# Performance work log

Measured on AMD Instinct MI355X. Metric: run time of the kernel, lower is better.

The kernel has to match this reference:

```python
import jax, jax.numpy as jnp
import numpy as np
import math

EMBED_DIM = 1024
NUM_HEADS = 16
HEAD_DIM = EMBED_DIM // NUM_HEADS          # 64
SUB_HEAD_DIM = HEAD_DIM // 2               # 32
SCALING = 1.0 / math.sqrt(SUB_HEAD_DIM)
LAMBDA_INIT = 0.8 - 0.6 * math.exp(-0.3 * 0)  # layer_idx = 0 -> 0.2


def setup_inputs() -> dict:
    key = jax.random.key(0)
    ks = jax.random.split(key, 10)
    B, T, D = 2, 2048, EMBED_DIM
    xav = math.sqrt(6.0 / (D + D))  # xavier_uniform bound for square-ish mats
    return {
        "query": jax.random.normal(ks[0], (B, T, D), jnp.float32),
        "key": jax.random.normal(ks[1], (B, T, D), jnp.float32),
        "value": jax.random.normal(ks[2], (B, T, D), jnp.float32),
        "in_proj_weight": jax.random.uniform(ks[3], (3 * D, D), jnp.float32, -xav, xav),
        "in_proj_bias": jnp.zeros((3 * D,), jnp.float32),
        "out_proj_weight": jax.random.uniform(ks[4], (D, D), jnp.float32, -xav, xav),
        "out_proj_bias": jnp.zeros((D,), jnp.float32),
        "lambda_q1": 0.1 * jax.random.normal(ks[5], (SUB_HEAD_DIM,), jnp.float32),
        "lambda_k1": 0.1 * jax.random.normal(ks[6], (SUB_HEAD_DIM,), jnp.float32),
        "lambda_q2": 0.1 * jax.random.normal(ks[7], (SUB_HEAD_DIM,), jnp.float32),
        "lambda_k2": 0.1 * jax.random.normal(ks[8], (SUB_HEAD_DIM,), jnp.float32),
    }


def reference(query, key, value, in_proj_weight, in_proj_bias,
              out_proj_weight, out_proj_bias,
              lambda_q1, lambda_k1, lambda_q2, lambda_k2):
    B, T, D = query.shape
    S = key.shape[1]
    H, hd, sd = NUM_HEADS, HEAD_DIM, SUB_HEAD_DIM

    qw, kw, vw = jnp.split(in_proj_weight, 3, axis=0)
    qb, kb, vb = jnp.split(in_proj_bias, 3, axis=0)
    q = query @ qw.T + qb
    k = key @ kw.T + kb
    v = value @ vw.T + vb

    # [B, H, T, head_dim]
    q = q.reshape(B, T, H, hd).transpose(0, 2, 1, 3)
    k = k.reshape(B, S, H, hd).transpose(0, 2, 1, 3)
    v = v.reshape(B, S, H, hd).transpose(0, 2, 1, 3)

    q1, q2 = q[..., :sd], q[..., sd:]
    k1, k2 = k[..., :sd], k[..., sd:]

    logits_1 = jnp.einsum('bhtd,bhsd->bhts', q1, k1) * SCALING
    logits_2 = jnp.einsum('bhtd,bhsd->bhts', q2, k2) * SCALING

    a1 = jax.nn.softmax(logits_1, axis=-1)
    a2 = jax.nn.softmax(logits_2, axis=-1)

    lam = (jnp.exp(jnp.dot(lambda_q1, lambda_k1))
           - jnp.exp(jnp.dot(lambda_q2, lambda_k2)) + LAMBDA_INIT)

    diff_weights = a1 - lam * a2
    attn_output = jnp.einsum('bhts,bhsd->bhtd', diff_weights, v)
    attn_output = attn_output * (1.0 - LAMBDA_INIT)

    attn_output = attn_output.transpose(0, 2, 1, 3).reshape(B, T, D)
    output = attn_output @ out_proj_weight.T + out_proj_bias
    return output
```

## Files before the change

### kernel.cpp

```cpp
#include <hip/hip_runtime.h>
#include <cstdint>
#include <cstddef>

typedef unsigned short u16;
typedef __attribute__((ext_vector_type(8))) short bf16x8;
typedef __attribute__((ext_vector_type(4))) short bf16x4;
typedef __attribute__((ext_vector_type(4))) float f32x4;

__device__ __forceinline__ u16 f2bf(float f) {
  uint32_t u = __float_as_uint(f);
  u += 0x7fffu + ((u >> 16) & 1u);
  return (u16)(u >> 16);
}

__device__ __forceinline__ short f2bfs(float f) {
  __bf16 h = (__bf16)f;
  return __builtin_bit_cast(short, h);
}

__device__ __forceinline__ float bf2f(u16 u) {
  return __uint_as_float(((uint32_t)u) << 16);
}

#define MFMA16(a, b, c) __builtin_amdgcn_mfma_f32_16x16x32_bf16((a), (b), (c), 0, 0, 0)

__device__ __forceinline__ float ex2(float x) {
#if __has_builtin(__builtin_amdgcn_exp2f)
  return __builtin_amdgcn_exp2f(x);
#else
  return exp2f(x);
#endif
}

__global__ __launch_bounds__(256) void cvt5_kernel(const float* __restrict__ q,
                                                   const float* __restrict__ k,
                                                   const float* __restrict__ v,
                                                   const float* __restrict__ w0,
                                                   const float* __restrict__ w1,
                                                   u16* __restrict__ X,
                                                   u16* __restrict__ Wqkv,
                                                   u16* __restrict__ Wout,
                                                   int n8i, int n8w, int n8o) {
  int i = blockIdx.x * blockDim.x + threadIdx.x;
  const int y = blockIdx.y;
  const float* src;
  u16* dst;
  if (y < 3) {
    if (i >= n8i) return;
    src = (y == 0) ? q : (y == 1 ? k : v);
    dst = X + (size_t)y * n8i * 8;
  } else if (y == 3) {
    if (i >= n8w) return;
    src = w0; dst = Wqkv;
  } else {
    if (i >= n8o) return;
    src = w1; dst = Wout;
  }
  const float4* p = (const float4*)src;
  float4 a = p[i * 2], b = p[i * 2 + 1];
  u16 o[8] = {f2bf(a.x), f2bf(a.y), f2bf(a.z), f2bf(a.w),
              f2bf(b.x), f2bf(b.y), f2bf(b.z), f2bf(b.w)};
  *(int4*)(dst + (size_t)i * 8) = *(const int4*)o;
}

__global__ __launch_bounds__(256) void gemm_qkv(const u16* __restrict__ Abase,
                                                const u16* __restrict__ B,
                                                const float* __restrict__ bias,
                                                u16* __restrict__ QH, u16* __restrict__ KH,
                                                u16* __restrict__ VT,
                                                int M, int N, int K) {
  __shared__ u16 As[128][68];
  __shared__ u16 Bs[128][68];
  const int nb = blockIdx.x, mb = blockIdx.y;
  const int t = threadIdx.x;
  const u16* A = Abase + (size_t)(nb >> 3) * (size_t)M * K;
  const int w = t >> 6, lane = t & 63;
  const int wr = w >> 1, wc = w & 1;
  const int lr = lane & 15, lk = lane >> 4;
  const f32x4 zero4 = {0.f, 0.f, 0.f, 0.f};
  f32x4 acc[4][4];
#pragma unroll
  for (int i = 0; i < 4; ++i)
#pragma unroll
    for (int j = 0; j < 4; ++j) acc[i][j] = zero4;

  const int srow = t >> 3;
  const int scol = (t & 7) << 3;
  const u16* Ap = A + (size_t)(mb * 128 + srow) * K + scol;
  const u16* Bp = B + (size_t)(nb * 128 + srow) * K + scol;

  for (int k0 = 0; k0 < K; k0 += 64) {
    __syncthreads();
#pragma unroll
    for (int j = 0; j < 4; ++j) {
      *(int4*)&As[srow + 32 * j][scol] = *(const int4*)(Ap + (size_t)(32 * j) * K + k0);
      *(int4*)&Bs[srow + 32 * j][scol] = *(const int4*)(Bp + (size_t)(32 * j) * K + k0);
    }
    __syncthreads();
#pragma unroll
    for (int kk = 0; kk < 2; ++kk) {
      bf16x8 af[4], bfr[4];
#pragma unroll
      for (int mf = 0; mf < 4; ++mf)
        af[mf] = *(const bf16x8*)&As[wr * 64 + mf * 16 + lr][kk * 32 + lk * 8];
#pragma unroll
      for (int nf = 0; nf < 4; ++nf)
        bfr[nf] = *(const bf16x8*)&Bs[wc * 64 + nf * 16 + lr][kk * 32 + lk * 8];
#pragma unroll
      for (int mf = 0; mf < 4; ++mf)
#pragma unroll
        for (int nf = 0; nf < 4; ++nf) acc[mf][nf] = MFMA16(af[mf], bfr[nf], acc[mf][nf]);
    }
  }

  const int third = nb >> 3;
  const int bb = mb >> 4;
#pragma unroll
  for (int nf = 0; nf < 4; ++nf) {
    const int col = nb * 128 + wc * 64 + nf * 16 + lr;
    const int c = col & 1023;
    const int h = c >> 6, d = c & 63;
    const float bv = bias[col];
    u16* qk = (third == 0 ? QH : KH) + (size_t)(bb * 16 + h) * 2048 * 64;
    u16* vt = VT + ((size_t)(bb * 16 + h) * 64 + d) * 2048;
#pragma unroll
    for (int mf = 0; mf < 4; ++mf) {
      const int row0 = mb * 128 + wr * 64 + mf * 16 + lk * 4;
      const int s0 = row0 & 2047;
      if (third < 2) {
#pragma unroll
        for (int r = 0; r < 4; ++r)
          qk[(size_t)(s0 + r) * 64 + d] = f2bf(acc[mf][nf][r] + bv);
      } else {
        u16 tmp[4];
#pragma unroll
        for (int r = 0; r < 4; ++r) tmp[r] = f2bf(acc[mf][nf][r] + bv);
        *(uint2*)&vt[s0] = *(const uint2*)tmp;
      }
    }
  }
}

__global__ __launch_bounds__(256) void gemm_out(const u16* __restrict__ A,
                                                const u16* __restrict__ B,
                                                const float* __restrict__ bias,
                                                float* __restrict__ C,
                                                int M, int N, int K) {
  __shared__ u16 As[128][68];
  __shared__ u16 Bs[64][68];
  const int nb = blockIdx.x, mb = blockIdx.y;
  const int t = threadIdx.x;
  const int w = t >> 6, lane = t & 63;
  const int lr = lane & 15, lk = lane >> 4;
  const f32x4 zero4 = {0.f, 0.f, 0.f, 0.f};
  f32x4 acc[2][4];
#pragma unroll
  for (int i = 0; i < 2; ++i)
#pragma unroll
    for (int j = 0; j < 4; ++j) acc[i][j] = zero4;

  const int srow = t >> 3;
  const int scol = (t & 7) << 3;
  const u16* Ap = A + (size_t)(mb * 128 + srow) * K + scol;
  const u16* Bp = B + (size_t)(nb * 64 + srow) * K + scol;

  for (int k0 = 0; k0 < K; k0 += 64) {
    __syncthreads();
#pragma unroll
    for (int j = 0; j < 4; ++j)
      *(int4*)&As[srow + 32 * j][scol] = *(const int4*)(Ap + (size_t)(32 * j) * K + k0);
#pragma unroll
    for (int j = 0; j < 2; ++j)
      *(int4*)&Bs[srow + 32 * j][scol] = *(const int4*)(Bp + (size_t)(32 * j) * K + k0);
    __syncthreads();
#pragma unroll
    for (int kk = 0; kk < 2; ++kk) {
      bf16x8 af[2], bfr[4];
#pragma unroll
      for (int mf = 0; mf < 2; ++mf)
        af[mf] = *(const bf16x8*)&As[w * 32 + mf * 16 + lr][kk * 32 + lk * 8];
#pragma unroll
      for (int nf = 0; nf < 4; ++nf)
        bfr[nf] = *(const bf16x8*)&Bs[nf * 16 + lr][kk * 32 + lk * 8];
#pragma unroll
      for (int mf = 0; mf < 2; ++mf)
#pragma unroll
        for (int nf = 0; nf < 4; ++nf) acc[mf][nf] = MFMA16(af[mf], bfr[nf], acc[mf][nf]);
    }
  }

#pragma unroll
  for (int nf = 0; nf < 4; ++nf) {
    const int col = nb * 64 + nf * 16 + lr;
    const float bv = bias[col];
#pragma unroll
    for (int mf = 0; mf < 2; ++mf) {
      const int row0 = mb * 128 + w * 32 + mf * 16 + lk * 4;
#pragma unroll
      for (int r = 0; r < 4; ++r)
        C[(size_t)(row0 + r) * N + col] = acc[mf][nf][r] + bv;
    }
  }
}

__global__ __launch_bounds__(512, 2) void diff_attn(const u16* __restrict__ QH,
                                                    const u16* __restrict__ KH,
                                                    const u16* __restrict__ VT,
                                                    const float* __restrict__ lq1,
                                                    const float* __restrict__ lk1,
                                                    const float* __restrict__ lq2,
                                                    const float* __restrict__ lk2,
                                                    u16* __restrict__ ATTN) {
  __shared__ u16 Ks[64][68];
  __shared__ u16 Vs[64][68];
  const int t = threadIdx.x;
  const int id = blockIdx.x;
  const int swz = (id & 7) * 64 + (id >> 3);
  const int qt = swz & 15, bh = swz >> 4;
  const int b = bh >> 4, h = bh & 15;
  const int w = t >> 6, lane = t & 63;
  const int lr = lane & 15, lk = lane >> 4;
  const float QSC = 0.17677669529663687f * 1.4426950408889634f;

  float dd1 = 0.f, dd2 = 0.f;
  for (int i = 0; i < 32; ++i) { dd1 += lq1[i] * lk1[i]; dd2 += lq2[i] * lk2[i]; }
  const float lam = __expf(dd1) - __expf(dd2) + 0.2f;

  const int srow = t >> 3;
  const int scol = (t & 7) << 3;
  const int krow = (srow & 32) | ((srow & 4) << 2) | ((srow & 24) >> 1) | (srow & 3);
  const u16* qh = QH + (size_t)(b * 16 + h) * 2048 * 64;
  const u16* kh = KH + (size_t)(b * 16 + h) * 2048 * 64;
  const u16* vt = VT + (size_t)(b * 16 + h) * 64 * 2048;

  bf16x8 qa[2];
#pragma unroll
  for (int hh = 0; hh < 2; ++hh) {
    bf16x8 q = *(const bf16x8*)(qh + (size_t)(qt * 128 + w * 16 + lr) * 64 + hh * 32 + lk * 8);
#pragma unroll
    for (int i = 0; i < 8; ++i) q[i] = f2bfs(bf2f((u16)q[i]) * QSC);
    qa[hh] = q;
  }

  const f32x4 zero4 = {0.f, 0.f, 0.f, 0.f};
  f32x4 O[2][4], Ol[2];
#pragma unroll
  for (int hh = 0; hh < 2; ++hh) {
    Ol[hh] = zero4;
#pragma unroll
    for (int df = 0; df < 4; ++df) O[hh][df] = zero4;
  }
  bf16x8 vone8;
#pragma unroll
  for (int i = 0; i < 8; ++i) vone8[i] = (short)0x3F80;

  const u16* kp = kh + (size_t)srow * 64 + scol;
  const u16* vp = vt + (size_t)srow * 2048 + scol;

  int4 kA = *(const int4*)kp;
  int4 vA = *(const int4*)vp;
  int4 kB, vB;

  for (int it = 0; it < 32; ++it) {
    __syncthreads();
    *(int4*)&Ks[krow][scol] = kA;
    *(int4*)&Vs[srow][scol] = vA;
    if (it < 31) {
      const int s1 = (it + 1) * 64;
      kB = *(const int4*)(kp + (size_t)s1 * 64);
      vB = *(const int4*)(vp + s1);
    }
    __syncthreads();

    bf16x8 pk8[2][2];
#pragma unroll
    for (int hh = 0; hh < 2; ++hh) {
      f32x4 St[4];
      __builtin_amdgcn_s_setprio(1);
#pragma unroll
      for (int nf = 0; nf < 4; ++nf) {
        bf16x8 kb = *(const bf16x8*)&Ks[nf * 16 + lr][hh * 32 + lk * 8];
        St[nf] = MFMA16(kb, qa[hh], zero4);
      }
      __builtin_amdgcn_s_setprio(0);
#pragma unroll
      for (int j = 0; j < 2; ++j) {
        bf16x8 p;
#pragma unroll
        for (int a = 0; a < 2; ++a)
#pragma unroll
          for (int r = 0; r < 4; ++r)
            p[a * 4 + r] = f2bfs(ex2(St[2 * j + a][r]));
        pk8[hh][j] = p;
      }
    }

    __builtin_amdgcn_s_setprio(1);
#pragma unroll
    for (int j = 0; j < 2; ++j) {
      const bf16x8 pa0 = pk8[0][j], pa1 = pk8[1][j];
#pragma unroll
      for (int df = 0; df < 4; ++df) {
        bf16x8 vb = *(const bf16x8*)&Vs[df * 16 + lr][j * 32 + lk * 8];
        O[0][df] = MFMA16(pa0, vb, O[0][df]);
        O[1][df] = MFMA16(pa1, vb, O[1][df]);
      }
      Ol[0] = MFMA16(pa0, vone8, Ol[0]);
      Ol[1] = MFMA16(pa1, vone8, Ol[1]);
    }
    __builtin_amdgcn_s_setprio(0);

    kA = kB; vA = vB;
  }

  float i1[4], i2[4];
#pragma unroll
  for (int r = 0; r < 4; ++r) {
    i1[r] = 1.f / Ol[0][r];
    i2[r] = 1.f / Ol[1][r];
  }
  const size_t qrow0 = (size_t)b * 2048 + (size_t)qt * 128;
#pragma unroll
  for (int df = 0; df < 4; ++df) {
    const int col = h * 64 + df * 16 + lr;
#pragma unroll
    for (int r = 0; r < 4; ++r) {
      const size_t row = qrow0 + w * 16 + lk * 4 + r;
      float v = 0.8f * (O[0][df][r] * i1[r] - lam * O[1][df][r] * i2[r]);
      ATTN[row * 1024 + col] = f2bf(v);
    }
  }
}

extern "C" void kernel_launch(void* const* d_in, const int* in_sizes, int n_in,
                              void* d_out, int out_size, void* d_ws, size_t ws_size,
                              hipStream_t stream) {
  (void)in_sizes; (void)n_in; (void)out_size; (void)ws_size;
  const float* query = (const float*)d_in[0];
  const float* key_  = (const float*)d_in[1];
  const float* value = (const float*)d_in[2];
  const float* ipw   = (const float*)d_in[3];
  const float* ipb   = (const float*)d_in[4];
  const float* opw   = (const float*)d_in[5];
  const float* opb   = (const float*)d_in[6];
  const float* lq1   = (const float*)d_in[7];
  const float* lk1   = (const float*)d_in[8];
  const float* lq2   = (const float*)d_in[9];
  const float* lk2   = (const float*)d_in[10];

  const int M = 4096, D = 1024;
  u16* X    = (u16*)d_ws;
  u16* Wqkv = X + (size_t)3 * M * D;
  u16* Wout = Wqkv + (size_t)3 * D * D;
  u16* QH   = Wout + (size_t)D * D;
  u16* KH   = QH + (size_t)M * D;
  u16* VT   = KH + (size_t)M * D;
  u16* ATTN = VT + (size_t)M * D;

  {
    int n8i = (int)((size_t)M * D / 8);
    int n8w = (int)((size_t)3 * D * D / 8);
    int n8o = (int)((size_t)D * D / 8);
    cvt5_kernel<<<dim3((n8i + 255) / 256, 5), dim3(256), 0, stream>>>(
        query, key_, value, ipw, opw, X, Wqkv, Wout, n8i, n8w, n8o);
  }

  gemm_qkv<<<dim3(24, 32), dim3(256), 0, stream>>>(
      X, Wqkv, ipb, QH, KH, VT, M, 3 * D, D);
  diff_attn<<<dim3(512), dim3(512), 0, stream>>>(QH, KH, VT, lq1, lk1, lq2, lk2, ATTN);
  gemm_out<<<dim3(16, 32), dim3(256), 0, stream>>>(
      ATTN, Wout, opb, (float*)d_out, M, D, D);
}
```

Baseline: 135.2 us.

## Use direct global-to-LDS loads in GEMMs and double attention KV tile

The QKV and output GEMMs now load tiles with global_load_lds, which writes straight into unpadded LDS instead of passing through registers, so the register round trip goes away. In exchange the LDS rows lose their padding and may suffer bank conflicts. The attention kernel now stages 128 keys per iteration instead of 64, which halves the number of barrier pairs and makes each prefetch larger, at the cost of more LDS and registers.

```diff
diff --git a/kernel.cpp b/kernel.cpp
--- a/kernel.cpp
+++ b/kernel.cpp
@@ -30,6 +30,12 @@
 #else
   return exp2f(x);
 #endif
+}
+
+__device__ __forceinline__ void gload_lds16(const u16* g, u16* l) {
+  __builtin_amdgcn_global_load_lds(
+      (const __attribute__((address_space(1))) unsigned int*)g,
+      (__attribute__((address_space(3))) unsigned int*)l, 16, 0, 0);
 }
 
 __global__ __launch_bounds__(256) void cvt5_kernel(const float* __restrict__ q,
@@ -69,8 +75,8 @@
                                                 u16* __restrict__ QH, u16* __restrict__ KH,
                                                 u16* __restrict__ VT,
                                                 int M, int N, int K) {
-  __shared__ u16 As[128][68];
-  __shared__ u16 Bs[128][68];
+  __shared__ u16 As[128 * 64];
+  __shared__ u16 Bs[128 * 64];
   const int nb = blockIdx.x, mb = blockIdx.y;
   const int t = threadIdx.x;
   const u16* A = Abase + (size_t)(nb >> 3) * (size_t)M * K;
@@ -84,17 +90,18 @@
 #pragma unroll
     for (int j = 0; j < 4; ++j) acc[i][j] = zero4;
 
-  const int srow = t >> 3;
-  const int scol = (t & 7) << 3;
-  const u16* Ap = A + (size_t)(mb * 128 + srow) * K + scol;
-  const u16* Bp = B + (size_t)(nb * 128 + srow) * K + scol;
+  const int grow = (w << 3) + (lane >> 3);
+  const int gcol = (lane & 7) << 3;
+  const u16* Ap = A + (size_t)(mb * 128 + grow) * K + gcol;
+  const u16* Bp = B + (size_t)(nb * 128 + grow) * K + gcol;
+  const int lbase = w << 9;
 
   for (int k0 = 0; k0 < K; k0 += 64) {
     __syncthreads();
 #pragma unroll
     for (int j = 0; j < 4; ++j) {
-      *(int4*)&As[srow + 32 * j][scol] = *(const int4*)(Ap + (size_t)(32 * j) * K + k0);
-      *(int4*)&Bs[srow + 32 * j][scol] = *(const int4*)(Bp + (size_t)(32 * j) * K + k0);
+      gload_lds16(Ap + (size_t)(j * 32) * K + k0, &As[j * 2048 + lbase]);
+      gload_lds16(Bp + (size_t)(j * 32) * K + k0, &Bs[j * 2048 + lbase]);
     }
     __syncthreads();
 #pragma unroll
@@ -102,10 +109,10 @@
       bf16x8 af[4], bfr[4];
 #pragma unroll
       for (int mf = 0; mf < 4; ++mf)
-        af[mf] = *(const bf16x8*)&As[wr * 64 + mf * 16 + lr][kk * 32 + lk * 8];
+        af[mf] = *(const bf16x8*)&As[(wr * 64 + mf * 16 + lr) * 64 + kk * 32 + lk * 8];
 #pragma unroll
       for (int nf = 0; nf < 4; ++nf)
-        bfr[nf] = *(const bf16x8*)&Bs[wc * 64 + nf * 16 + lr][kk * 32 + lk * 8];
+        bfr[nf] = *(const bf16x8*)&Bs[(wc * 64 + nf * 16 + lr) * 64 + kk * 32 + lk * 8];
 #pragma unroll
       for (int mf = 0; mf < 4; ++mf)
 #pragma unroll
@@ -146,8 +153,8 @@
                                                 const float* __restrict__ bias,
                                                 float* __restrict__ C,
                                                 int M, int N, int K) {
-  __shared__ u16 As[128][68];
-  __shared__ u16 Bs[64][68];
+  __shared__ u16 As[128 * 64];
+  __shared__ u16 Bs[64 * 64];
   const int nb = blockIdx.x, mb = blockIdx.y;
   const int t = threadIdx.x;
   const int w = t >> 6, lane = t & 63;
@@ -159,29 +166,30 @@
 #pragma unroll
     for (int j = 0; j < 4; ++j) acc[i][j] = zero4;
 
-  const int srow = t >> 3;
-  const int scol = (t & 7) << 3;
-  const u16* Ap = A + (size_t)(mb * 128 + srow) * K + scol;
-  const u16* Bp = B + (size_t)(nb * 64 + srow) * K + scol;
+  const int grow = (w << 3) + (lane >> 3);
+  const int gcol = (lane & 7) << 3;
+  const u16* Ap = A + (size_t)(mb * 128 + grow) * K + gcol;
+  const u16* Bp = B + (size_t)(nb * 64 + grow) * K + gcol;
+  const int lbase = w << 9;
 
   for (int k0 = 0; k0 < K; k0 += 64) {
     __syncthreads();
 #pragma unroll
     for (int j = 0; j < 4; ++j)
-      *(int4*)&As[srow + 32 * j][scol] = *(const int4*)(Ap + (size_t)(32 * j) * K + k0);
+      gload_lds16(Ap + (size_t)(j * 32) * K + k0, &As[j * 2048 + lbase]);
 #pragma unroll
     for (int j = 0; j < 2; ++j)
-      *(int4*)&Bs[srow + 32 * j][scol] = *(const int4*)(Bp + (size_t)(32 * j) * K + k0);
+      gload_lds16(Bp + (size_t)(j * 32) * K + k0, &Bs[j * 2048 + lbase]);
     __syncthreads();
 #pragma unroll
     for (int kk = 0; kk < 2; ++kk) {
       bf16x8 af[2], bfr[4];
 #pragma unroll
       for (int mf = 0; mf < 2; ++mf)
-        af[mf] = *(const bf16x8*)&As[w * 32 + mf * 16 + lr][kk * 32 + lk * 8];
+        af[mf] = *(const bf16x8*)&As[(w * 32 + mf * 16 + lr) * 64 + kk * 32 + lk * 8];
 #pragma unroll
       for (int nf = 0; nf < 4; ++nf)
-        bfr[nf] = *(const bf16x8*)&Bs[nf * 16 + lr][kk * 32 + lk * 8];
+        bfr[nf] = *(const bf16x8*)&Bs[(nf * 16 + lr) * 64 + kk * 32 + lk * 8];
 #pragma unroll
       for (int mf = 0; mf < 2; ++mf)
 #pragma unroll
@@ -211,8 +219,8 @@
                                                     const float* __restrict__ lq2,
                                                     const float* __restrict__ lk2,
                                                     u16* __restrict__ ATTN) {
-  __shared__ u16 Ks[64][68];
-  __shared__ u16 Vs[64][68];
+  __shared__ u16 Ks[128][68];
+  __shared__ u16 Vs[64][136];
   const int t = threadIdx.x;
   const int id = blockIdx.x;
   const int swz = (id & 7) * 64 + (id >> 3);
@@ -257,60 +265,69 @@
   const u16* kp = kh + (size_t)srow * 64 + scol;
   const u16* vp = vt + (size_t)srow * 2048 + scol;
 
-  int4 kA = *(const int4*)kp;
-  int4 vA = *(const int4*)vp;
-  int4 kB, vB;
-
-  for (int it = 0; it < 32; ++it) {
-    __syncthreads();
-    *(int4*)&Ks[krow][scol] = kA;
-    *(int4*)&Vs[srow][scol] = vA;
-    if (it < 31) {
-      const int s1 = (it + 1) * 64;
-      kB = *(const int4*)(kp + (size_t)s1 * 64);
-      vB = *(const int4*)(vp + s1);
-    }
-    __syncthreads();
-
-    bf16x8 pk8[2][2];
-#pragma unroll
-    for (int hh = 0; hh < 2; ++hh) {
-      f32x4 St[4];
+  int4 kA0 = *(const int4*)kp;
+  int4 kA1 = *(const int4*)(kp + (size_t)64 * 64);
+  int4 vA0 = *(const int4*)vp;
+  int4 vA1 = *(const int4*)(vp + 64);
+  int4 kB0, kB1, vB0, vB1;
+
+  for (int it = 0; it < 16; ++it) {
+    __syncthreads();
+    *(int4*)&Ks[krow][scol]        = kA0;
+    *(int4*)&Ks[krow + 64][scol]   = kA1;
+    *(int4*)&Vs[srow][scol]        = vA0;
+    *(int4*)&Vs[srow][scol + 64]   = vA1;
+    if (it < 15) {
+      const int s1 = (it + 1) * 128;
+      kB0 = *(const int4*)(kp + (size_t)s1 * 64);
+      kB1 = *(const int4*)(kp + (size_t)(s1 + 64) * 64);
+      vB0 = *(const int4*)(vp + s1);
+      vB1 = *(const int4*)(vp + s1 + 64);
+    }
+    __syncthreads();
+
+#pragma unroll
+    for (int sub = 0; sub < 2; ++sub) {
+      bf16x8 pk8[2][2];
+#pragma unroll
+      for (int hh = 0; hh < 2; ++hh) {
+        f32x4 St[4];
+        __builtin_amdgcn_s_setprio(1);
+#pragma unroll
+        for (int nf = 0; nf < 4; ++nf) {
+          bf16x8 kb = *(const bf16x8*)&Ks[sub * 64 + nf * 16 + lr][hh * 32 + lk * 8];
+          St[nf] = MFMA16(kb, qa[hh], zero4);
+        }
+        __builtin_amdgcn_s_setprio(0);
+#pragma unroll
+        for (int j = 0; j < 2; ++j) {
+          bf16x8 p;
+#pragma unroll
+          for (int a = 0; a < 2; ++a)
+#pragma unroll
+            for (int r = 0; r < 4; ++r)
+              p[a * 4 + r] = f2bfs(ex2(St[2 * j + a][r]));
+          pk8[hh][j] = p;
+        }
+      }
+
       __builtin_amdgcn_s_setprio(1);
 #pragma unroll
-      for (int nf = 0; nf < 4; ++nf) {
-        bf16x8 kb = *(const bf16x8*)&Ks[nf * 16 + lr][hh * 32 + lk * 8];
-        St[nf] = MFMA16(kb, qa[hh], zero4);
+      for (int j = 0; j < 2; ++j) {
+        const bf16x8 pa0 = pk8[0][j], pa1 = pk8[1][j];
+#pragma unroll
+        for (int df = 0; df < 4; ++df) {
+          bf16x8 vb = *(const bf16x8*)&Vs[df * 16 + lr][sub * 64 + j * 32 + lk * 8];
+          O[0][df] = MFMA16(pa0, vb, O[0][df]);
+          O[1][df] = MFMA16(pa1, vb, O[1][df]);
+        }
+        Ol[0] = MFMA16(pa0, vone8, Ol[0]);
+        Ol[1] = MFMA16(pa1, vone8, Ol[1]);
       }
       __builtin_amdgcn_s_setprio(0);
-#pragma unroll
-      for (int j = 0; j < 2; ++j) {
-        bf16x8 p;
-#pragma unroll
-        for (int a = 0; a < 2; ++a)
-#pragma unroll
-          for (int r = 0; r < 4; ++r)
-            p[a * 4 + r] = f2bfs(ex2(St[2 * j + a][r]));
-        pk8[hh][j] = p;
-      }
-    }
-
-    __builtin_amdgcn_s_setprio(1);
-#pragma unroll
-    for (int j = 0; j < 2; ++j) {
-      const bf16x8 pa0 = pk8[0][j], pa1 = pk8[1][j];
-#pragma unroll
-      for (int df = 0; df < 4; ++df) {
-        bf16x8 vb = *(const bf16x8*)&Vs[df * 16 + lr][j * 32 + lk * 8];
-        O[0][df] = MFMA16(pa0, vb, O[0][df]);
-        O[1][df] = MFMA16(pa1, vb, O[1][df]);
-      }
-      Ol[0] = MFMA16(pa0, vone8, Ol[0]);
-      Ol[1] = MFMA16(pa1, vone8, Ol[1]);
-    }
-    __builtin_amdgcn_s_setprio(0);
-
-    kA = kB; vA = vB;
+    }
+
+    kA0 = kB0; kA1 = kB1; vA0 = vB0; vA1 = vB1;
   }
 
   float i1[4], i2[4];
```

New measurement: 146.7 us. +8.5%, slower.
